# Kernel optimization log

Hardware: AMD Instinct MI355X
Metric: run time of the kernel (lower is better)

## Reference

```python
import jax, jax.numpy as jnp
import numpy as np

# 27 kernel taps x 3 offset components (dz, dy, dx), matching the module's offset0 list.
OFFSET0 = np.array([
    1, 1, 1, 1, 1, 0, 1, 1, -1, 1, 0, 1, 1, 0, 0, 1, 0, -1, 1, -1, 1, 1, -1, 0, 1, -1, -1,
    0, 1, 1, 0, 1, 0, 0, 1, -1, 0, 0, 1, 0, 0, 0, 0, 0, -1, 0, -1, 1, 0, -1, 0, 0, -1, -1,
    -1, 1, 1, -1, 1, 0, -1, 1, -1, -1, 0, 1, -1, 0, 0, -1, 0, -1, -1, -1, 1, -1, -1, 0, -1, -1, -1
], dtype=np.float64).reshape(27, 3)

BN_EPS = 1e-5


def upsample_nearest2(x):
    # nn.Upsample(scale_factor=2), default mode='nearest', on [B,C,Z,Y,X]
    x = jnp.repeat(x, 2, axis=2)
    x = jnp.repeat(x, 2, axis=3)
    return jnp.repeat(x, 2, axis=4)


def deform_conv3d_static(x, W, b, alpha):
    """3D deformable conv, kernel 3, pad 1, stride 1, with spatially-constant
    per-tap offsets alpha*OFFSET0. Zero padding outside; trilinear sampling.
    Since offsets are static, each tap samples at a fixed fractional shift,
    implemented as a static trilinear combination of slices of the padded input.
    x: [B,C,Z,Y,X], W: [O,C,3,3,3], b: [O].
    """
    B, C, Z, Y, X = x.shape
    # pad 2: 1 for the 3x3x3 kernel + 1 for fractional offsets (|alpha*d| <= 0.7)
    xp = jnp.pad(x, ((0, 0), (0, 0), (2, 2), (2, 2), (2, 2)))
    out = None
    t = 0
    for kz in range(3):
        for ky in range(3):
            for kx in range(3):
                dz, dy, dx = (alpha * OFFSET0[t]).tolist()
                s = (kz - 1 + dz, ky - 1 + dy, kx - 1 + dx)  # shift rel. to output voxel
                f = [int(np.floor(v)) for v in s]
                w = [v - fl for v, fl in zip(s, f)]
                vol = None
                for cz in (0, 1):
                    for cy in (0, 1):
                        for cx in (0, 1):
                            wt = ((w[0] if cz else 1.0 - w[0]) *
                                  (w[1] if cy else 1.0 - w[1]) *
                                  (w[2] if cx else 1.0 - w[2]))
                            if wt == 0.0:
                                continue
                            z0 = 2 + f[0] + cz
                            y0 = 2 + f[1] + cy
                            x0 = 2 + f[2] + cx
                            sl = xp[:, :, z0:z0 + Z, y0:y0 + Y, x0:x0 + X]
                            sl = jnp.float32(wt) * sl
                            vol = sl if vol is None else vol + sl
                contrib = jnp.einsum('oc,bczyx->bozyx', W[:, :, kz, ky, kx], vol)
                out = contrib if out is None else out + contrib
                t += 1
    return out + b[None, :, None, None, None]


def batchnorm(x, g, bt, m, v):
    # eval-mode BatchNorm3d over channel axis 1
    inv = g * jax.lax.rsqrt(v + BN_EPS)
    return x * inv[None, :, None, None, None] + (bt - m * inv)[None, :, None, None, None]


def setup_inputs() -> dict:
    key = jax.random.key(0)
    ks = jax.random.split(key, 13)
    ch_in, ch_out = 64, 32
    x = jax.random.normal(ks[0], (1, ch_in, 32, 32, 32), jnp.float32)
    w_def = jax.random.normal(ks[1], (ch_out, ch_in, 3, 3, 3), jnp.float32) * 0.05
    b_def = jax.random.normal(ks[2], (ch_out,), jnp.float32) * 0.05
    bn1_g = 1.0 + 0.1 * jax.random.normal(ks[3], (ch_out,), jnp.float32)
    bn1_b = 0.1 * jax.random.normal(ks[4], (ch_out,), jnp.float32)
    bn1_m = 0.1 * jax.random.normal(ks[5], (ch_out,), jnp.float32)
    bn1_v = jax.random.uniform(ks[6], (ch_out,), jnp.float32, 0.5, 1.5)
    w_comb = jax.random.normal(ks[7], (ch_out, 3 * ch_out), jnp.float32) * 0.1
    b_comb = 0.05 * jax.random.normal(ks[8], (ch_out,), jnp.float32)
    bn2_g = 1.0 + 0.1 * jax.random.normal(ks[9], (ch_out,), jnp.float32)
    bn2_b = 0.1 * jax.random.normal(ks[10], (ch_out,), jnp.float32)
    bn2_m = 0.1 * jax.random.normal(ks[11], (ch_out,), jnp.float32)
    bn2_v = jax.random.uniform(ks[12], (ch_out,), jnp.float32, 0.5, 1.5)
    return {"x": x, "w_def": w_def, "b_def": b_def,
            "bn1_g": bn1_g, "bn1_b": bn1_b, "bn1_m": bn1_m, "bn1_v": bn1_v,
            "w_comb": w_comb, "b_comb": b_comb,
            "bn2_g": bn2_g, "bn2_b": bn2_b, "bn2_m": bn2_m, "bn2_v": bn2_v}


def reference(x, w_def, b_def, bn1_g, bn1_b, bn1_m, bn1_v,
              w_comb, b_comb, bn2_g, bn2_b, bn2_m, bn2_v):
    xu = upsample_nearest2(x)
    branches = []
    for alpha in (0.0, 0.4, 0.7):  # shared deform-conv weights, three static offset scales
        o = deform_conv3d_static(xu, w_def, b_def, alpha)
        o = jax.nn.relu(batchnorm(o, bn1_g, bn1_b, bn1_m, bn1_v))
        branches.append(o)
    cat = jnp.concatenate(branches, axis=1)  # [B, 3*ch_out, Z,Y,X]
    y = jnp.einsum('oc,bczyx->bozyx', w_comb, cat) + b_comb[None, :, None, None, None]
    y = batchnorm(y, bn2_g, bn2_b, bn2_m, bn2_v)
    return jax.nn.relu(y)
```

## Files before the change

### kernel.cpp

```cpp
#include <hip/hip_runtime.h>


typedef __bf16 bf16x8 __attribute__((ext_vector_type(8)));
typedef float f32x16 __attribute__((ext_vector_type(16)));
typedef unsigned u32x2 __attribute__((ext_vector_type(2)));

__device__ inline unsigned short f2bf(float f) {
  unsigned int u = __float_as_uint(f);
  u += 0x7FFFu + ((u >> 16) & 1u);
  return (unsigned short)(u >> 16);
}

__device__ inline bf16x8 bc16(uint4 v) { return __builtin_bit_cast(bf16x8, v); }

__device__ inline unsigned cvtpk(float lo, float hi) {
  unsigned r;
  asm("v_cvt_pk_bf16_f32 %0, %1, %2" : "=v"(r) : "v"(lo), "v"(hi));
  return r;
}

__device__ inline void plswap(unsigned& a, unsigned& b) {
  u32x2 r = __builtin_amdgcn_permlane32_swap(a, b, false, false);
  a = r.x;
  b = r.y;
}

__device__ inline void gload16(const unsigned short* g, unsigned short* l) {
  __builtin_amdgcn_global_load_lds(
      (const __attribute__((address_space(1))) unsigned int*)(const void*)g,
      (__attribute__((address_space(3))) unsigned int*)(void*)l, 16, 0, 0);
}

__device__ inline float ucoef(int abit, int k, int jbit, float alpha) {
  if (abit == 0) return (k == 0) ? (jbit ? alpha : 1.f - alpha) : (jbit ? 1.f : 0.f);
  return (k == 2) ? (jbit ? 1.f - alpha : alpha) : (jbit ? 0.f : 1.f);
}

#define XREG_USH 524352
#define XREG_B 1048704
#define XZERO_B 1048576u

__global__ void k_prep(const float* __restrict__ x, unsigned short* __restrict__ xT2,
                       const float* __restrict__ w_def, const float* __restrict__ bn1_g,
                       const float* __restrict__ bn1_v, unsigned short* __restrict__ W_sw,
                       const float* __restrict__ w_comb, const float* __restrict__ b_comb,
                       const float* __restrict__ bn2_g, const float* __restrict__ bn2_b,
                       const float* __restrict__ bn2_m, const float* __restrict__ bn2_v,
                       const float* __restrict__ b_def, const float* __restrict__ bn1_b,
                       const float* __restrict__ bn1_m, unsigned short* __restrict__ W2_sw,
                       float* __restrict__ bias1, float* __restrict__ bias2) {
  __shared__ unsigned short t[64][65];
  int bid = blockIdx.x;
  if (bid < 512) {
    int s0 = bid * 64;
    int lane = threadIdx.x & 63;
    int grp = threadIdx.x >> 6;
#pragma unroll
    for (int c = grp; c < 64; c += 4)
      t[c][lane] = f2bf(x[c * 32768 + s0 + lane]);
    __syncthreads();
    int q = lane >> 4, e = lane & 15;
#pragma unroll
    for (int s = grp; s < 64; s += 4)
      xT2[q * XREG_USH + (size_t)(s0 + s) * 16 + e] = t[lane][s];
  } else if (bid < 2048) {
    int e = (bid - 512) * 256 + threadIdx.x;
    int j = e & 7;
    int lane = (e >> 3) & 63;
    int idx = e >> 9;
    int nt = idx % 3;
    idx /= 3;
    int s = idx & 31;
    int p = idx >> 5;
    int o = lane & 31;
    int br = nt;
    int kk = 16 * s + ((lane >> 5) << 3) + j;
    int tap = kk >> 6, ch = kk & 63;
    int jz = (tap >> 2) & 1, jy = (tap >> 1) & 1, jx = tap & 1;
    int a = (p >> 2) & 1, b = (p >> 1) & 1, cp = p & 1;
    float alpha = (br == 0) ? 0.f : ((br == 1) ? 0.4f : 0.7f);
    const float* wb = w_def + (o * 64 + ch) * 27;
    float sum = 0.f;
    for (int kz = 0; kz < 3; ++kz) {
      float uz = ucoef(a, kz, jz, alpha);
      if (uz == 0.f) continue;
      for (int ky = 0; ky < 3; ++ky) {
        float uy = ucoef(b, ky, jy, alpha);
        if (uy == 0.f) continue;
        float uzy = uz * uy;
        for (int kx = 0; kx < 3; ++kx) {
          float ux = ucoef(cp, kx, jx, alpha);
          if (ux != 0.f) sum += wb[kz * 9 + ky * 3 + kx] * uzy * ux;
        }
      }
    }
    float s1 = bn1_g[o] * rsqrtf(bn1_v[o] + 1e-5f);
    W_sw[e] = f2bf(sum * s1);
  } else {
    int tid = threadIdx.x;
    for (int e = tid; e < 3072; e += 256) {
      int j = e & 7;
      int lane = (e >> 3) & 63;
      int s2 = e >> 9;
      int n = lane & 31;
      int k = 16 * s2 + ((lane >> 5) << 3) + j;
      float sc2 = bn2_g[n] * rsqrtf(bn2_v[n] + 1e-5f);
      W2_sw[e] = f2bf(w_comb[n * 96 + k] * sc2);
    }
    {
      int q = tid >> 6, e2 = tid & 63;
      xT2[q * XREG_USH + 524288 + e2] = 0;
    }
    if (tid < 32) {
      float s1 = bn1_g[tid] * rsqrtf(bn1_v[tid] + 1e-5f);
      bias1[tid] = (b_def[tid] - bn1_m[tid]) * s1 + bn1_b[tid];
      float s2 = bn2_g[tid] * rsqrtf(bn2_v[tid] + 1e-5f);
      bias2[tid] = (b_comb[tid] - bn2_m[tid]) * s2 + bn2_b[tid];
    }
  }
}

__launch_bounds__(128, 3)
__global__ void k_main(const unsigned short* __restrict__ xT2,
                       const unsigned short* __restrict__ W_sw,
                       const unsigned short* __restrict__ W2_sw,
                       const float* __restrict__ bias1f,
                       const float* __restrict__ bias2f,
                       float* __restrict__ out) {
  __shared__ unsigned short wring[2][6144];
  __shared__ float blds[64];
  int tid = threadIdx.x;
  int lane = tid & 63;
  int wv = tid >> 6;
  int bid = blockIdx.x;
  int tb = (bid & 7) | ((bid >> 5) << 3);
  int ph = (bid >> 3) & 3;
  int bph = ph & 1, a = ph >> 1;
  int tx = tb & 3, ty = (tb >> 2) & 7, tz = tb >> 5;
  int i0 = tz * 4, j0 = ty * 4, k0 = tx * 8;

  if (tid < 32) {
    blds[tid] = bias1f[tid];
    blds[32 + tid] = bias2f[tid];
  }

  int m = lane & 31, h = lane >> 5;
  int ax = m & 7, ay = (m >> 3) & 1, az = (m >> 4) & 1;
  int p0 = (a << 2) | (bph << 1);
  int zbase = i0 + 2 * wv + az;
  const char* xb0 = (const char*)xT2 + (h << 4);

  auto stage = [&](int c) {
    int pn = p0 | (c >> 3);
    const unsigned short* g =
        W_sw + pn * 49152 + (c & 7) * 6144 + wv * 3072 + lane * 8;
    unsigned short* l = &wring[c & 1][wv * 3072];
#pragma unroll
    for (int k = 0; k < 6; ++k) gload16(g + k * 512, l + k * 512);
  };

  __syncthreads();
  stage(0);

  unsigned osvp[2][8];
  f32x16 acc[2][3];
#pragma unroll
  for (int mt = 0; mt < 2; ++mt)
#pragma unroll
    for (int nt = 0; nt < 3; ++nt) acc[mt][nt] = (f32x16)0.f;

  const uint4* w2q = (const uint4*)W2_sw + lane;

  for (int c = 0; c < 16; ++c) {
    asm volatile("s_waitcnt vmcnt(0)" ::: "memory");
    __builtin_amdgcn_s_barrier();
    __builtin_amdgcn_sched_barrier(0);
    if (c < 15) stage(c + 1);
    __builtin_amdgcn_sched_barrier(0);

    int cp = c >> 3, tap = c & 7;
    int jz = (tap >> 2) & 1, jy = (tap >> 1) & 1, jx = tap & 1;
    int gz = zbase + a - 1 + jz;
    int gx = k0 + ax + cp - 1 + jx;
    bool okzx = ((unsigned)gz < 32u) && ((unsigned)gx < 32u);
    unsigned xo[2];
#pragma unroll
    for (int mt = 0; mt < 2; ++mt) {
      int gy = j0 + 2 * mt + ay + bph - 1 + jy;
      bool ok = okzx && ((unsigned)gy < 32u);
      unsigned off = (unsigned)(((gz * 32 + gy) * 32 + gx) * 32);
      xo[mt] = ok ? off : XZERO_B;
    }

    const unsigned short* wfb = &wring[c & 1][lane * 8];
#pragma unroll
    for (int q = 0; q < 4; ++q) {
      const char* xp = xb0 + q * XREG_B;
      bf16x8 a0 = bc16(*(const uint4*)(xp + xo[0]));
      bf16x8 a1 = bc16(*(const uint4*)(xp + xo[1]));
      const unsigned short* wf = wfb + q * 1536;
      bf16x8 bb0 = bc16(*(const uint4*)(wf));
      bf16x8 bb1 = bc16(*(const uint4*)(wf + 512));
      bf16x8 bb2 = bc16(*(const uint4*)(wf + 1024));
      __builtin_amdgcn_s_setprio(1);
      acc[0][0] = __builtin_amdgcn_mfma_f32_32x32x16_bf16(bb0, a0, acc[0][0], 0, 0, 0);
      acc[1][0] = __builtin_amdgcn_mfma_f32_32x32x16_bf16(bb0, a1, acc[1][0], 0, 0, 0);
      acc[0][1] = __builtin_amdgcn_mfma_f32_32x32x16_bf16(bb1, a0, acc[0][1], 0, 0, 0);
      acc[1][1] = __builtin_amdgcn_mfma_f32_32x32x16_bf16(bb1, a1, acc[1][1], 0, 0, 0);
      acc[0][2] = __builtin_amdgcn_mfma_f32_32x32x16_bf16(bb2, a0, acc[0][2], 0, 0, 0);
      acc[1][2] = __builtin_amdgcn_mfma_f32_32x32x16_bf16(bb2, a1, acc[1][2], 0, 0, 0);
      __builtin_amdgcn_s_setprio(0);
    }

    if (c == 7) {
#pragma unroll
      for (int mt = 0; mt < 2; ++mt) {
        f32x16 acc2 = (f32x16)0.f;
#pragma unroll
        for (int nt = 0; nt < 3; ++nt) {
          unsigned ww[8];
#pragma unroll
          for (int qc = 0; qc < 8; ++qc) {
            int q = qc >> 1, c2 = qc & 1;
            int r0 = 4 * q + 2 * c2;
            int row = (r0 & 3) + ((r0 >> 2) << 3) + (h << 2);
            float lo = fmaxf(acc[mt][nt][r0] + blds[row], 0.f);
            float hi = fmaxf(acc[mt][nt][r0 + 1] + blds[row + 1], 0.f);
            ww[2 * q + c2] = cvtpk(lo, hi);
          }
          plswap(ww[0], ww[2]);
          plswap(ww[1], ww[3]);
          plswap(ww[4], ww[6]);
          plswap(ww[5], ww[7]);
          uint4 frA = make_uint4(ww[0], ww[1], ww[2], ww[3]);
          uint4 frB = make_uint4(ww[4], ww[5], ww[6], ww[7]);
          acc2 = __builtin_amdgcn_mfma_f32_32x32x16_bf16(bc16(w2q[(2 * nt) * 64]),
                                                         bc16(frA), acc2, 0, 0, 0);
          acc2 = __builtin_amdgcn_mfma_f32_32x32x16_bf16(bc16(w2q[(2 * nt + 1) * 64]),
                                                         bc16(frB), acc2, 0, 0, 0);
        }
#pragma unroll
        for (int w = 0; w < 8; ++w) {
          int r0 = 2 * w;
          int row = (r0 & 3) + ((r0 >> 2) << 3) + (h << 2);
          float o0 = fmaxf(acc2[r0] + blds[32 + row], 0.f);
          float o1 = fmaxf(acc2[r0 + 1] + blds[32 + row + 1], 0.f);
          osvp[mt][w] = cvtpk(o0, o1);
        }
#pragma unroll
        for (int nt = 0; nt < 3; ++nt) acc[mt][nt] = (f32x16)0.f;
      }
    }
  }

#pragma unroll
  for (int mt = 0; mt < 2; ++mt) {
    f32x16 acc2 = (f32x16)0.f;
#pragma unroll
    for (int nt = 0; nt < 3; ++nt) {
      unsigned ww[8];
#pragma unroll
      for (int qc = 0; qc < 8; ++qc) {
        int q = qc >> 1, c2 = qc & 1;
        int r0 = 4 * q + 2 * c2;
        int row = (r0 & 3) + ((r0 >> 2) << 3) + (h << 2);
        float lo = fmaxf(acc[mt][nt][r0] + blds[row], 0.f);
        float hi = fmaxf(acc[mt][nt][r0 + 1] + blds[row + 1], 0.f);
        ww[2 * q + c2] = cvtpk(lo, hi);
      }
      plswap(ww[0], ww[2]);
      plswap(ww[1], ww[3]);
      plswap(ww[4], ww[6]);
      plswap(ww[5], ww[7]);
      uint4 frA = make_uint4(ww[0], ww[1], ww[2], ww[3]);
      uint4 frB = make_uint4(ww[4], ww[5], ww[6], ww[7]);
      acc2 = __builtin_amdgcn_mfma_f32_32x32x16_bf16(bc16(w2q[(2 * nt) * 64]),
                                                     bc16(frA), acc2, 0, 0, 0);
      acc2 = __builtin_amdgcn_mfma_f32_32x32x16_bf16(bc16(w2q[(2 * nt + 1) * 64]),
                                                     bc16(frB), acc2, 0, 0, 0);
    }
    int Z = 2 * zbase + a;
    int Y = 2 * (j0 + 2 * mt + ay) + bph;
    size_t sb = ((size_t)Z << 11) + (Y << 5) + (k0 + ax);
    float2* o2 = (float2*)out;
#pragma unroll
    for (int r = 0; r < 16; ++r) {
      int ch = (r & 3) + ((r >> 2) << 3) + (h << 2);
      float v1 = fmaxf(acc2[r] + blds[32 + ch], 0.f);
      unsigned pw = osvp[mt][r >> 1];
      float pv = __uint_as_float((r & 1) ? (pw & 0xffff0000u) : (pw << 16));
      o2[((size_t)ch << 17) + sb] = make_float2(pv, v1);
    }
  }
}

extern "C" void kernel_launch(void* const* d_in, const int* in_sizes, int n_in,
                              void* d_out, int out_size, void* d_ws, size_t ws_size,
                              hipStream_t stream) {
  (void)in_sizes; (void)n_in; (void)out_size; (void)ws_size;
  const float* x      = (const float*)d_in[0];
  const float* w_def  = (const float*)d_in[1];
  const float* b_def  = (const float*)d_in[2];
  const float* bn1_g  = (const float*)d_in[3];
  const float* bn1_b  = (const float*)d_in[4];
  const float* bn1_m  = (const float*)d_in[5];
  const float* bn1_v  = (const float*)d_in[6];
  const float* w_comb = (const float*)d_in[7];
  const float* b_comb = (const float*)d_in[8];
  const float* bn2_g  = (const float*)d_in[9];
  const float* bn2_b  = (const float*)d_in[10];
  const float* bn2_m  = (const float*)d_in[11];
  const float* bn2_v  = (const float*)d_in[12];

  char* ws = (char*)d_ws;
  unsigned short* xT2  = (unsigned short*)(ws);
  unsigned short* W_sw = (unsigned short*)(ws + 4194816);
  unsigned short* W2sw = (unsigned short*)(ws + 4981248);
  float* bias1 = (float*)(ws + 4987392);
  float* bias2 = (float*)(ws + 4987520);
  float* out = (float*)d_out;

  hipLaunchKernelGGL(k_prep, dim3(2049), dim3(256), 0, stream,
                     x, xT2, w_def, bn1_g, bn1_v, W_sw,
                     w_comb, b_comb, bn2_g, bn2_b, bn2_m, bn2_v,
                     b_def, bn1_b, bn1_m, W2sw, bias1, bias2);
  hipLaunchKernelGGL(k_main, dim3(1024), dim3(128), 0, stream,
                     xT2, W_sw, W2sw, bias1, bias2, out);
}
```

Before: 58.08 us.

## Load full per-phase weight set into LDS once with larger 512-thread blocks

Each block now handles a single output parity phase (including the x parity) and preloads all 8 taps of that phase's weights (96 KB) into LDS up front, replacing the double-buffered per-tap streaming ring and its per-iteration barriers. Blocks grow to 8 waves covering an 8x8x8 input tile, and the grid halves to 512 blocks. Each output is written once as a single float rather than as paired float2 stores of two phases, which removes the mid-loop epilogue and the bf16 stash of the first phase. The trade-off is a large LDS footprint that limits blocks per CU, a serialized weight load before any compute, and narrower stores.

```diff
diff --git a/kernel.cpp b/kernel.cpp
--- a/kernel.cpp
+++ b/kernel.cpp
@@ -120,79 +120,66 @@
   }
 }
 
-__launch_bounds__(128, 3)
+__launch_bounds__(512, 2)
 __global__ void k_main(const unsigned short* __restrict__ xT2,
                        const unsigned short* __restrict__ W_sw,
                        const unsigned short* __restrict__ W2_sw,
                        const float* __restrict__ bias1f,
                        const float* __restrict__ bias2f,
                        float* __restrict__ out) {
-  __shared__ unsigned short wring[2][6144];
+  __shared__ unsigned short wlds[49152];
   __shared__ float blds[64];
   int tid = threadIdx.x;
   int lane = tid & 63;
   int wv = tid >> 6;
   int bid = blockIdx.x;
-  int tb = (bid & 7) | ((bid >> 5) << 3);
-  int ph = (bid >> 3) & 3;
-  int bph = ph & 1, a = ph >> 1;
-  int tx = tb & 3, ty = (tb >> 2) & 7, tz = tb >> 5;
-  int i0 = tz * 4, j0 = ty * 4, k0 = tx * 8;
-
+  int tb = bid & 63;
+  int p = bid >> 6;
+  int cp = p & 1, bph = (p >> 1) & 1, a = p >> 2;
+  int tx = tb & 3, ty = (tb >> 2) & 3, tz = tb >> 4;
+  int i0 = tz * 8, j0 = ty * 8, k0 = tx * 8;
+
+  {
+    const unsigned short* g = W_sw + (size_t)p * 49152 + wv * 6144 + lane * 8;
+    unsigned short* l = wlds + wv * 6144;
+#pragma unroll
+    for (int k = 0; k < 12; ++k) gload16(g + k * 512, l + k * 512);
+  }
   if (tid < 32) {
     blds[tid] = bias1f[tid];
     blds[32 + tid] = bias2f[tid];
   }
+  __syncthreads();
 
   int m = lane & 31, h = lane >> 5;
-  int ax = m & 7, ay = (m >> 3) & 1, az = (m >> 4) & 1;
-  int p0 = (a << 2) | (bph << 1);
-  int zbase = i0 + 2 * wv + az;
+  int ax = m & 7, ay = (m >> 3) & 1, az = m >> 4;
+  int zs = wv >> 2, ys = wv & 3;
+  int zin0 = i0 + 4 * zs + az;
+  int yin = j0 + 2 * ys + ay;
   const char* xb0 = (const char*)xT2 + (h << 4);
 
-  auto stage = [&](int c) {
-    int pn = p0 | (c >> 3);
-    const unsigned short* g =
-        W_sw + pn * 49152 + (c & 7) * 6144 + wv * 3072 + lane * 8;
-    unsigned short* l = &wring[c & 1][wv * 3072];
-#pragma unroll
-    for (int k = 0; k < 6; ++k) gload16(g + k * 512, l + k * 512);
-  };
-
-  __syncthreads();
-  stage(0);
-
-  unsigned osvp[2][8];
   f32x16 acc[2][3];
 #pragma unroll
   for (int mt = 0; mt < 2; ++mt)
 #pragma unroll
     for (int nt = 0; nt < 3; ++nt) acc[mt][nt] = (f32x16)0.f;
 
-  const uint4* w2q = (const uint4*)W2_sw + lane;
-
-  for (int c = 0; c < 16; ++c) {
-    asm volatile("s_waitcnt vmcnt(0)" ::: "memory");
-    __builtin_amdgcn_s_barrier();
-    __builtin_amdgcn_sched_barrier(0);
-    if (c < 15) stage(c + 1);
-    __builtin_amdgcn_sched_barrier(0);
-
-    int cp = c >> 3, tap = c & 7;
+#pragma unroll
+  for (int tap = 0; tap < 8; ++tap) {
     int jz = (tap >> 2) & 1, jy = (tap >> 1) & 1, jx = tap & 1;
-    int gz = zbase + a - 1 + jz;
+    int gz0 = zin0 + a - 1 + jz;
+    int gy = yin + bph - 1 + jy;
     int gx = k0 + ax + cp - 1 + jx;
-    bool okzx = ((unsigned)gz < 32u) && ((unsigned)gx < 32u);
+    bool okyx = ((unsigned)gy < 32u) && ((unsigned)gx < 32u);
     unsigned xo[2];
 #pragma unroll
     for (int mt = 0; mt < 2; ++mt) {
-      int gy = j0 + 2 * mt + ay + bph - 1 + jy;
-      bool ok = okzx && ((unsigned)gy < 32u);
+      int gz = gz0 + 2 * mt;
+      bool ok = okyx && ((unsigned)gz < 32u);
       unsigned off = (unsigned)(((gz * 32 + gy) * 32 + gx) * 32);
       xo[mt] = ok ? off : XZERO_B;
     }
-
-    const unsigned short* wfb = &wring[c & 1][lane * 8];
+    const unsigned short* wfb = wlds + tap * 6144 + lane * 8;
 #pragma unroll
     for (int q = 0; q < 4; ++q) {
       const char* xp = xb0 + q * XREG_B;
@@ -202,57 +189,16 @@
       bf16x8 bb0 = bc16(*(const uint4*)(wf));
       bf16x8 bb1 = bc16(*(const uint4*)(wf + 512));
       bf16x8 bb2 = bc16(*(const uint4*)(wf + 1024));
-      __builtin_amdgcn_s_setprio(1);
       acc[0][0] = __builtin_amdgcn_mfma_f32_32x32x16_bf16(bb0, a0, acc[0][0], 0, 0, 0);
       acc[1][0] = __builtin_amdgcn_mfma_f32_32x32x16_bf16(bb0, a1, acc[1][0], 0, 0, 0);
       acc[0][1] = __builtin_amdgcn_mfma_f32_32x32x16_bf16(bb1, a0, acc[0][1], 0, 0, 0);
       acc[1][1] = __builtin_amdgcn_mfma_f32_32x32x16_bf16(bb1, a1, acc[1][1], 0, 0, 0);
       acc[0][2] = __builtin_amdgcn_mfma_f32_32x32x16_bf16(bb2, a0, acc[0][2], 0, 0, 0);
       acc[1][2] = __builtin_amdgcn_mfma_f32_32x32x16_bf16(bb2, a1, acc[1][2], 0, 0, 0);
-      __builtin_amdgcn_s_setprio(0);
-    }
-
-    if (c == 7) {
-#pragma unroll
-      for (int mt = 0; mt < 2; ++mt) {
-        f32x16 acc2 = (f32x16)0.f;
-#pragma unroll
-        for (int nt = 0; nt < 3; ++nt) {
-          unsigned ww[8];
-#pragma unroll
-          for (int qc = 0; qc < 8; ++qc) {
-            int q = qc >> 1, c2 = qc & 1;
-            int r0 = 4 * q + 2 * c2;
-            int row = (r0 & 3) + ((r0 >> 2) << 3) + (h << 2);
-            float lo = fmaxf(acc[mt][nt][r0] + blds[row], 0.f);
-            float hi = fmaxf(acc[mt][nt][r0 + 1] + blds[row + 1], 0.f);
-            ww[2 * q + c2] = cvtpk(lo, hi);
-          }
-          plswap(ww[0], ww[2]);
-          plswap(ww[1], ww[3]);
-          plswap(ww[4], ww[6]);
-          plswap(ww[5], ww[7]);
-          uint4 frA = make_uint4(ww[0], ww[1], ww[2], ww[3]);
-          uint4 frB = make_uint4(ww[4], ww[5], ww[6], ww[7]);
-          acc2 = __builtin_amdgcn_mfma_f32_32x32x16_bf16(bc16(w2q[(2 * nt) * 64]),
-                                                         bc16(frA), acc2, 0, 0, 0);
-          acc2 = __builtin_amdgcn_mfma_f32_32x32x16_bf16(bc16(w2q[(2 * nt + 1) * 64]),
-                                                         bc16(frB), acc2, 0, 0, 0);
-        }
-#pragma unroll
-        for (int w = 0; w < 8; ++w) {
-          int r0 = 2 * w;
-          int row = (r0 & 3) + ((r0 >> 2) << 3) + (h << 2);
-          float o0 = fmaxf(acc2[r0] + blds[32 + row], 0.f);
-          float o1 = fmaxf(acc2[r0 + 1] + blds[32 + row + 1], 0.f);
-          osvp[mt][w] = cvtpk(o0, o1);
-        }
-#pragma unroll
-        for (int nt = 0; nt < 3; ++nt) acc[mt][nt] = (f32x16)0.f;
-      }
-    }
-  }
-
+    }
+  }
+
+  const uint4* w2q = (const uint4*)W2_sw + lane;
 #pragma unroll
   for (int mt = 0; mt < 2; ++mt) {
     f32x16 acc2 = (f32x16)0.f;
@@ -279,17 +225,14 @@
       acc2 = __builtin_amdgcn_mfma_f32_32x32x16_bf16(bc16(w2q[(2 * nt + 1) * 64]),
                                                      bc16(frB), acc2, 0, 0, 0);
     }
-    int Z = 2 * zbase + a;
-    int Y = 2 * (j0 + 2 * mt + ay) + bph;
-    size_t sb = ((size_t)Z << 11) + (Y << 5) + (k0 + ax);
-    float2* o2 = (float2*)out;
+    int Z = 2 * (zin0 + 2 * mt) + a;
+    int Y = 2 * yin + bph;
+    int X = 2 * (k0 + ax) + cp;
+    size_t sb = ((size_t)Z << 12) + (Y << 6) + X;
 #pragma unroll
     for (int r = 0; r < 16; ++r) {
       int ch = (r & 3) + ((r >> 2) << 3) + (h << 2);
-      float v1 = fmaxf(acc2[r] + blds[32 + ch], 0.f);
-      unsigned pw = osvp[mt][r >> 1];
-      float pv = __uint_as_float((r & 1) ? (pw & 0xffff0000u) : (pw << 16));
-      o2[((size_t)ch << 17) + sb] = make_float2(pv, v1);
+      out[((size_t)ch << 18) + sb] = fmaxf(acc2[r] + blds[32 + ch], 0.f);
     }
   }
 }
@@ -324,6 +267,6 @@
                      x, xT2, w_def, bn1_g, bn1_v, W_sw,
                      w_comb, b_comb, bn2_g, bn2_b, bn2_m, bn2_v,
                      b_def, bn1_b, bn1_m, W2sw, bias1, bias2);
-  hipLaunchKernelGGL(k_main, dim3(1024), dim3(128), 0, stream,
+  hipLaunchKernelGGL(k_main, dim3(512), dim3(512), 0, stream,
                      xT2, W_sw, W2sw, bias1, bias2, out);
 }
```

Result: no change. 57.44 us (-1.1%).
